# Kernel optimization log

Hardware: AMD Instinct MI355X
Metric: run time of the kernel (lower is better)

Reference implementation:

```python
import jax, jax.numpy as jnp
import numpy as np

RMS_EPS = 1e-6

def rms_norm(x, w, eps=RMS_EPS):
    # LLaMA RMSNorm: x * rsqrt(mean(x^2) + eps) * w
    var = jnp.mean(jnp.square(x), axis=-1, keepdims=True)
    return x * jax.lax.rsqrt(var + eps) * w

def setup_inputs() -> dict:
    key = jax.random.key(0)
    k1, k2, k3 = jax.random.split(key, 3)
    B, S, D, V = 2, 2048, 4096, 32000
    hidden_states = jax.random.normal(k1, (B, S, D), dtype=jnp.float32)
    norm_weight = jnp.ones((D,), dtype=jnp.float32)
    lm_head_weight = jax.random.normal(k2, (V, D), dtype=jnp.float32) * 0.02
    attention_mask = jnp.ones((B, S), dtype=jnp.int32)
    labels = jax.random.randint(k3, (B, S), 0, V, dtype=jnp.int32).astype(jnp.int64)
    return {
        "hidden_states": hidden_states,
        "norm_weight": norm_weight,
        "lm_head_weight": lm_head_weight,
        "attention_mask": attention_mask,
        "labels": labels,
    }

def reference(hidden_states, norm_weight, lm_head_weight, attention_mask, labels):
    B, S, D = hidden_states.shape
    V = lm_head_weight.shape[0]
    h = rms_norm(hidden_states, norm_weight)
    # lm_head: Linear(D -> V, bias=False); cast logits to fp32 (full-vocab tensor)
    logits = jnp.einsum('bsd,vd->bsv', h, lm_head_weight).astype(jnp.float32)
    # shift: drop last logit position / first label position.
    # attention_mask is all-ones here, so the boolean select keeps every row
    # -> static-shape flatten to [B*(S-1), V], matching torch semantics.
    shift_logits = logits[:, :-1, :].reshape(B * (S - 1), V)
    shift_labels = labels[:, 1:].reshape(B * (S - 1))
    return shift_logits, shift_labels
```

## Files before the change

kernel.cpp:

```cpp
#include <hip/hip_runtime.h>
#include <hip/hip_bf16.h>
#include <stdint.h>

#define B_DIM 2
#define S_DIM 2048
#define D_DIM 4096
#define V_DIM 32000
#define M_DIM (B_DIM * S_DIM)
#define OUT_ROWS (B_DIM * (S_DIM-1))

typedef __hip_bfloat16 bf16;
typedef __bf16 bf16x8 __attribute__((ext_vector_type(8)));
typedef float floatx4 __attribute__((ext_vector_type(4)));

__device__ __forceinline__ void async16(const bf16* g, bf16* l) {
    __builtin_amdgcn_global_load_lds(
        (const __attribute__((address_space(1))) void*)g,
        (__attribute__((address_space(3))) void*)l,
        16, 0, 0);
}

__global__ void rmsnorm_cast_kernel(const float* __restrict__ x,
                                    const float* __restrict__ w,
                                    bf16* __restrict__ h) {
    const int row = blockIdx.x;
    const int t = threadIdx.x;
    const float* xr = x + (size_t)row * D_DIM;

    float4 vals[4];
    float ss = 0.f;
#pragma unroll
    for (int i = 0; i < 4; ++i) {
        float4 v = ((const float4*)xr)[t + i * 256];
        vals[i] = v;
        ss += v.x * v.x + v.y * v.y + v.z * v.z + v.w * v.w;
    }
#pragma unroll
    for (int off = 32; off; off >>= 1) ss += __shfl_down(ss, off, 64);
    __shared__ float wsum[4];
    const int lane = t & 63, wv = t >> 6;
    if (lane == 0) wsum[wv] = ss;
    __syncthreads();
    const float var = (wsum[0] + wsum[1] + wsum[2] + wsum[3]) * (1.0f / D_DIM);
    const float scale = rsqrtf(var + 1e-6f);

    bf16* hr = h + (size_t)row * D_DIM;
#pragma unroll
    for (int i = 0; i < 4; ++i) {
        const int f4 = t + i * 256;
        float4 v = vals[i];
        float4 wv4 = ((const float4*)w)[f4];
        ushort4 pk;
        bf16 b0 = __float2bfloat16(v.x * scale * wv4.x);
        bf16 b1 = __float2bfloat16(v.y * scale * wv4.y);
        bf16 b2 = __float2bfloat16(v.z * scale * wv4.z);
        bf16 b3 = __float2bfloat16(v.w * scale * wv4.w);
        pk.x = *(unsigned short*)&b0;
        pk.y = *(unsigned short*)&b1;
        pk.z = *(unsigned short*)&b2;
        pk.w = *(unsigned short*)&b3;
        ((ushort4*)hr)[f4] = pk;
    }
}

__global__ void wcast_kernel(const float* __restrict__ W, bf16* __restrict__ Wb) {
    const size_t i = (size_t)blockIdx.x * 256 + threadIdx.x;
    float4 v = ((const float4*)W)[i];
    ushort4 pk;
    bf16 b0 = __float2bfloat16(v.x);
    bf16 b1 = __float2bfloat16(v.y);
    bf16 b2 = __float2bfloat16(v.z);
    bf16 b3 = __float2bfloat16(v.w);
    pk.x = *(unsigned short*)&b0;
    pk.y = *(unsigned short*)&b1;
    pk.z = *(unsigned short*)&b2;
    pk.w = *(unsigned short*)&b3;
    ((ushort4*)Wb)[i] = pk;
}

#define BM 256
#define BN 256
#define BK 64

#define STAGE_A(db, half, kt) do { \
    const bf16* _g = aRow0 + (size_t)(half) * 128 * D_DIM + (kt) * BK; \
    bf16* _l = lds + (db) * 32768 + (half) * 8192 + t * 8; \
    async16(_g, _l); \
    async16(_g + (size_t)64 * D_DIM, _l + 4096); \
} while (0)

#define STAGE_B(db, half, kt) do { \
    const bf16* _g = bRow0 + (size_t)(half) * 128 * D_DIM + (kt) * BK; \
    bf16* _l = lds + (db) * 32768 + 16384 + (half) * 8192 + t * 8; \
    async16(_g, _l); \
    async16(_g + (size_t)64 * D_DIM, _l + 4096); \
} while (0)

#define LDA(db, mi, ks) (*(const bf16x8*)(lds + (db) * 32768 + aBase + (mi) * 1024 + ((ks) ? csw1 : csw0)))
#define LDB(db, ni, ks) (*(const bf16x8*)(lds + (db) * 32768 + bBase + (ni) * 1024 + ((ks) ? csw1 : csw0)))
#define MFMA(a, b, c) __builtin_amdgcn_mfma_f32_16x16x32_bf16((a), (b), (c), 0, 0, 0)
#define BAR() __builtin_amdgcn_s_barrier()
#define PRIO1() __builtin_amdgcn_s_setprio(1)
#define PRIO0() __builtin_amdgcn_s_setprio(0)

__global__ __launch_bounds__(512, 2) void gemm_kernel(const bf16* __restrict__ A,
                                                      const bf16* __restrict__ Bw,
                                                      float* __restrict__ Cout) {
    __shared__ __align__(16) bf16 lds[65536];

    const int bid = blockIdx.x;
    const int wg  = (bid & 7) * 250 + (bid >> 3);
    const int bm  = wg & 15;
    const int bn  = wg >> 4;
    const int m0  = bm * BM, n0 = bn * BN;

    const int t    = threadIdx.x;
    const int lane = t & 63;
    const int wv   = t >> 6;
    const int wmi  = wv >> 2;
    const int wni  = wv & 3;
    const int quad = lane >> 4;
    const int l15  = lane & 15;

    const int r0 = t >> 3;
    const int c0 = ((t & 7) ^ (r0 & 7)) << 3;
    const bf16* aRow0 = A  + (size_t)(m0 + r0) * D_DIM + c0;
    const bf16* bRow0 = Bw + (size_t)(n0 + r0) * D_DIM + c0;

    const int vx   = (l15 & 7) << 3;
    const int csw0 = ((quad << 3)     ) ^ vx;
    const int csw1 = ((quad << 3) | 32) ^ vx;
    const int aBase = wmi * 8192 + l15 * 64;
    const int bBase = 16384 + (wni >> 1) * 8192 + (wni & 1) * 4096 + l15 * 64;

    floatx4 acc[8][4] = {};
    bf16x8 af[4][2], b01[2][2], b23[2][2];

    STAGE_B(0, 0, 0); STAGE_B(0, 1, 0); STAGE_A(0, 0, 0); STAGE_A(0, 1, 0);
    STAGE_B(1, 0, 1); STAGE_B(1, 1, 1); STAGE_A(1, 0, 1); STAGE_A(1, 1, 1);
    asm volatile("s_waitcnt vmcnt(8)" ::: "memory");
    BAR();

    for (int it = 0; it < 32; ++it) {
        int kta = 2 * it + 2; if (kta > 63) kta = 63;
        int ktb = 2 * it + 3; if (ktb > 63) ktb = 63;

#pragma unroll
        for (int db = 0; db < 2; ++db) {
#pragma unroll
            for (int mi = 0; mi < 4; ++mi) { af[mi][0] = LDA(db, mi, 0); af[mi][1] = LDA(db, mi, 1); }
#pragma unroll
            for (int ni = 0; ni < 2; ++ni) { b01[ni][0] = LDB(db, ni, 0); b01[ni][1] = LDB(db, ni, 1); }
            if (db == 1) STAGE_A(0, 0, kta);
            BAR();
            PRIO1();
#pragma unroll
            for (int mi = 0; mi < 4; ++mi)
#pragma unroll
                for (int ni = 0; ni < 2; ++ni) {
                    acc[mi][ni] = MFMA(af[mi][0], b01[ni][0], acc[mi][ni]);
                    acc[mi][ni] = MFMA(af[mi][1], b01[ni][1], acc[mi][ni]);
                }
            PRIO0();
            BAR();

#pragma unroll
            for (int ni = 0; ni < 2; ++ni) { b23[ni][0] = LDB(db, ni + 2, 0); b23[ni][1] = LDB(db, ni + 2, 1); }
            if (db == 1) STAGE_A(0, 1, kta);
            BAR();
            PRIO1();
#pragma unroll
            for (int mi = 0; mi < 4; ++mi)
#pragma unroll
                for (int ni = 0; ni < 2; ++ni) {
                    acc[mi][ni + 2] = MFMA(af[mi][0], b23[ni][0], acc[mi][ni + 2]);
                    acc[mi][ni + 2] = MFMA(af[mi][1], b23[ni][1], acc[mi][ni + 2]);
                }
            PRIO0();
            BAR();

#pragma unroll
            for (int mi = 0; mi < 4; ++mi) { af[mi][0] = LDA(db, mi + 4, 0); af[mi][1] = LDA(db, mi + 4, 1); }
            if (db == 0) { STAGE_B(0, 0, kta); }
            else         { STAGE_B(1, 0, ktb); STAGE_B(1, 1, ktb); }
            BAR();
            PRIO1();
#pragma unroll
            for (int mi = 0; mi < 4; ++mi)
#pragma unroll
                for (int ni = 0; ni < 2; ++ni) {
                    acc[mi + 4][ni] = MFMA(af[mi][0], b01[ni][0], acc[mi + 4][ni]);
                    acc[mi + 4][ni] = MFMA(af[mi][1], b01[ni][1], acc[mi + 4][ni]);
                }
            PRIO0();
            BAR();

            if (db == 0) { STAGE_B(0, 1, kta); }
            else         { STAGE_A(1, 0, ktb); STAGE_A(1, 1, ktb); }
            BAR();
            PRIO1();
#pragma unroll
            for (int mi = 0; mi < 4; ++mi)
#pragma unroll
                for (int ni = 0; ni < 2; ++ni) {
                    acc[mi + 4][ni + 2] = MFMA(af[mi][0], b23[ni][0], acc[mi + 4][ni + 2]);
                    acc[mi + 4][ni + 2] = MFMA(af[mi][1], b23[ni][1], acc[mi + 4][ni + 2]);
                }
            PRIO0();
            if (db == 0) { asm volatile("s_waitcnt vmcnt(4)" ::: "memory"); }
            else         { asm volatile("s_waitcnt vmcnt(8)" ::: "memory"); }
            BAR();
        }
    }

    const int mbase = m0 + wmi * 128 + quad * 4;
    const int nbase = n0 + wni * 64 + l15;
#pragma unroll
    for (int mi = 0; mi < 8; ++mi) {
#pragma unroll
        for (int r = 0; r < 4; ++r) {
            const int m = mbase + mi * 16 + r;
            const int s = m & (S_DIM - 1);
            if (s == S_DIM - 1) continue;
            float* cp = Cout + (size_t)((m >> 11) * (S_DIM - 1) + s) * V_DIM + nbase;
#pragma unroll
            for (int ni = 0; ni < 4; ++ni)
                cp[ni * 16] = acc[mi][ni][r];
        }
    }
}

__global__ void labels_kernel(const int* __restrict__ labels, float* __restrict__ out) {
    const int r = blockIdx.x * 256 + threadIdx.x;
    if (r >= OUT_ROWS) return;
    const int b = r / (S_DIM - 1);
    const int s = r % (S_DIM - 1);
    out[r] = (float)labels[b * S_DIM + s + 1];
}

extern "C" void kernel_launch(void* const* d_in, const int* in_sizes, int n_in,
                              void* d_out, int out_size, void* d_ws, size_t ws_size,
                              hipStream_t stream) {
    const float* x      = (const float*)d_in[0];
    const float* nw     = (const float*)d_in[1];
    const float* W      = (const float*)d_in[2];
    const int*   labels = (const int*)d_in[4];

    float* logits_out = (float*)d_out;
    float* labels_out = logits_out + (size_t)OUT_ROWS * V_DIM;

    bf16* h  = (bf16*)d_ws;
    bf16* Wb = h + (size_t)M_DIM * D_DIM;

    rmsnorm_cast_kernel<<<M_DIM, 256, 0, stream>>>(x, nw, h);
    wcast_kernel<<<(int)((size_t)V_DIM * D_DIM / 4 / 256), 256, 0, stream>>>(W, Wb);
    gemm_kernel<<<(M_DIM / BM) * (V_DIM / BN), 512, 0, stream>>>(h, Wb, logits_out);
    labels_kernel<<<(OUT_ROWS + 255) / 256, 256, 0, stream>>>(labels, labels_out);
}
```

Measured before the change: 2.328 ms.

## Restructure GEMM mainloop with double-buffered A and triple-buffered B tiles

Replaces the combined double-buffered LDS layout with separate rings: two slots for the A tile and three for the B tile, each holding a full 256x64 tile. The loop now steps one K-tile per iteration and issues all loads for that iteration in its last phase. The B tile is fetched three tiles ahead and A two ahead, with a single vmcnt wait per iteration. This aims to hide more global-load latency. In exchange, LDS use grows to the full 160KB per block and the loads are bunched into one phase instead of spread across the four MFMA phases.

```diff
diff --git a/kernel.cpp b/kernel.cpp
--- a/kernel.cpp
+++ b/kernel.cpp
@@ -81,23 +81,28 @@
 #define BM 256
 #define BN 256
 #define BK 64
-
-#define STAGE_A(db, half, kt) do { \
-    const bf16* _g = aRow0 + (size_t)(half) * 128 * D_DIM + (kt) * BK; \
-    bf16* _l = lds + (db) * 32768 + (half) * 8192 + t * 8; \
-    async16(_g, _l); \
-    async16(_g + (size_t)64 * D_DIM, _l + 4096); \
+#define LDS_TILE 16384
+
+#define STAGE_A(slot, kt) do { \
+    const bf16* _g = aRow0 + (size_t)(kt) * BK; \
+    bf16* _l = ldsA + (slot) * LDS_TILE + t * 8; \
+    async16(_g,                       _l); \
+    async16(_g + (size_t) 64 * D_DIM, _l + 4096); \
+    async16(_g + (size_t)128 * D_DIM, _l + 8192); \
+    async16(_g + (size_t)192 * D_DIM, _l + 12288); \
 } while (0)
 
-#define STAGE_B(db, half, kt) do { \
-    const bf16* _g = bRow0 + (size_t)(half) * 128 * D_DIM + (kt) * BK; \
-    bf16* _l = lds + (db) * 32768 + 16384 + (half) * 8192 + t * 8; \
-    async16(_g, _l); \
-    async16(_g + (size_t)64 * D_DIM, _l + 4096); \
+#define STAGE_B(slot, kt) do { \
+    const bf16* _g = bRow0 + (size_t)(kt) * BK; \
+    bf16* _l = ldsB + (slot) * LDS_TILE + t * 8; \
+    async16(_g,                       _l); \
+    async16(_g + (size_t) 64 * D_DIM, _l + 4096); \
+    async16(_g + (size_t)128 * D_DIM, _l + 8192); \
+    async16(_g + (size_t)192 * D_DIM, _l + 12288); \
 } while (0)
 
-#define LDA(db, mi, ks) (*(const bf16x8*)(lds + (db) * 32768 + aBase + (mi) * 1024 + ((ks) ? csw1 : csw0)))
-#define LDB(db, ni, ks) (*(const bf16x8*)(lds + (db) * 32768 + bBase + (ni) * 1024 + ((ks) ? csw1 : csw0)))
+#define LDA(mi, ks) (*(const bf16x8*)(aT + (mi) * 1024 + aBase + ((ks) ? csw1 : csw0)))
+#define LDB(ni, ks) (*(const bf16x8*)(bT + (ni) * 1024 + bBase + ((ks) ? csw1 : csw0)))
 #define MFMA(a, b, c) __builtin_amdgcn_mfma_f32_16x16x32_bf16((a), (b), (c), 0, 0, 0)
 #define BAR() __builtin_amdgcn_s_barrier()
 #define PRIO1() __builtin_amdgcn_s_setprio(1)
@@ -106,7 +111,8 @@
 __global__ __launch_bounds__(512, 2) void gemm_kernel(const bf16* __restrict__ A,
                                                       const bf16* __restrict__ Bw,
                                                       float* __restrict__ Cout) {
-    __shared__ __align__(16) bf16 lds[65536];
+    __shared__ __align__(16) bf16 ldsA[2 * LDS_TILE];
+    __shared__ __align__(16) bf16 ldsB[3 * LDS_TILE];
 
     const int bid = blockIdx.x;
     const int wg  = (bid & 7) * 250 + (bid >> 3);
@@ -131,86 +137,87 @@
     const int csw0 = ((quad << 3)     ) ^ vx;
     const int csw1 = ((quad << 3) | 32) ^ vx;
     const int aBase = wmi * 8192 + l15 * 64;
-    const int bBase = 16384 + (wni >> 1) * 8192 + (wni & 1) * 4096 + l15 * 64;
+    const int bBase = (wni >> 1) * 8192 + (wni & 1) * 4096 + l15 * 64;
 
     floatx4 acc[8][4] = {};
     bf16x8 af[4][2], b01[2][2], b23[2][2];
 
-    STAGE_B(0, 0, 0); STAGE_B(0, 1, 0); STAGE_A(0, 0, 0); STAGE_A(0, 1, 0);
-    STAGE_B(1, 0, 1); STAGE_B(1, 1, 1); STAGE_A(1, 0, 1); STAGE_A(1, 1, 1);
-    asm volatile("s_waitcnt vmcnt(8)" ::: "memory");
+    STAGE_B(0, 0);
+    STAGE_A(0, 0);
+    STAGE_B(1, 1);
+    STAGE_A(1, 1);
+    STAGE_B(2, 2);
+    asm volatile("s_waitcnt vmcnt(12)" ::: "memory");
     BAR();
 
-    for (int it = 0; it < 32; ++it) {
-        int kta = 2 * it + 2; if (kta > 63) kta = 63;
-        int ktb = 2 * it + 3; if (ktb > 63) ktb = 63;
-
-#pragma unroll
-        for (int db = 0; db < 2; ++db) {
-#pragma unroll
-            for (int mi = 0; mi < 4; ++mi) { af[mi][0] = LDA(db, mi, 0); af[mi][1] = LDA(db, mi, 1); }
-#pragma unroll
-            for (int ni = 0; ni < 2; ++ni) { b01[ni][0] = LDB(db, ni, 0); b01[ni][1] = LDB(db, ni, 1); }
-            if (db == 1) STAGE_A(0, 0, kta);
-            BAR();
-            PRIO1();
-#pragma unroll
-            for (int mi = 0; mi < 4; ++mi)
-#pragma unroll
-                for (int ni = 0; ni < 2; ++ni) {
-                    acc[mi][ni] = MFMA(af[mi][0], b01[ni][0], acc[mi][ni]);
-                    acc[mi][ni] = MFMA(af[mi][1], b01[ni][1], acc[mi][ni]);
-                }
-            PRIO0();
-            BAR();
-
-#pragma unroll
-            for (int ni = 0; ni < 2; ++ni) { b23[ni][0] = LDB(db, ni + 2, 0); b23[ni][1] = LDB(db, ni + 2, 1); }
-            if (db == 1) STAGE_A(0, 1, kta);
-            BAR();
-            PRIO1();
-#pragma unroll
-            for (int mi = 0; mi < 4; ++mi)
-#pragma unroll
-                for (int ni = 0; ni < 2; ++ni) {
-                    acc[mi][ni + 2] = MFMA(af[mi][0], b23[ni][0], acc[mi][ni + 2]);
-                    acc[mi][ni + 2] = MFMA(af[mi][1], b23[ni][1], acc[mi][ni + 2]);
-                }
-            PRIO0();
-            BAR();
-
-#pragma unroll
-            for (int mi = 0; mi < 4; ++mi) { af[mi][0] = LDA(db, mi + 4, 0); af[mi][1] = LDA(db, mi + 4, 1); }
-            if (db == 0) { STAGE_B(0, 0, kta); }
-            else         { STAGE_B(1, 0, ktb); STAGE_B(1, 1, ktb); }
-            BAR();
-            PRIO1();
-#pragma unroll
-            for (int mi = 0; mi < 4; ++mi)
-#pragma unroll
-                for (int ni = 0; ni < 2; ++ni) {
-                    acc[mi + 4][ni] = MFMA(af[mi][0], b01[ni][0], acc[mi + 4][ni]);
-                    acc[mi + 4][ni] = MFMA(af[mi][1], b01[ni][1], acc[mi + 4][ni]);
-                }
-            PRIO0();
-            BAR();
-
-            if (db == 0) { STAGE_B(0, 1, kta); }
-            else         { STAGE_A(1, 0, ktb); STAGE_A(1, 1, ktb); }
-            BAR();
-            PRIO1();
-#pragma unroll
-            for (int mi = 0; mi < 4; ++mi)
-#pragma unroll
-                for (int ni = 0; ni < 2; ++ni) {
-                    acc[mi + 4][ni + 2] = MFMA(af[mi][0], b23[ni][0], acc[mi + 4][ni + 2]);
-                    acc[mi + 4][ni + 2] = MFMA(af[mi][1], b23[ni][1], acc[mi + 4][ni + 2]);
-                }
-            PRIO0();
-            if (db == 0) { asm volatile("s_waitcnt vmcnt(4)" ::: "memory"); }
-            else         { asm volatile("s_waitcnt vmcnt(8)" ::: "memory"); }
-            BAR();
-        }
+    int bs = 0;
+    for (int j = 0; j < 64; ++j) {
+        const int as = j & 1;
+        int ka = j + 2; if (ka > 63) ka = 63;
+        int kb = j + 3; if (kb > 63) kb = 63;
+        const bf16* aT = ldsA + as * LDS_TILE;
+        const bf16* bT = ldsB + bs * LDS_TILE;
+
+#pragma unroll
+        for (int mi = 0; mi < 4; ++mi) { af[mi][0] = LDA(mi, 0); af[mi][1] = LDA(mi, 1); }
+#pragma unroll
+        for (int ni = 0; ni < 2; ++ni) { b01[ni][0] = LDB(ni, 0); b01[ni][1] = LDB(ni, 1); }
+        BAR();
+        PRIO1();
+#pragma unroll
+        for (int mi = 0; mi < 4; ++mi)
+#pragma unroll
+            for (int ni = 0; ni < 2; ++ni) {
+                acc[mi][ni] = MFMA(af[mi][0], b01[ni][0], acc[mi][ni]);
+                acc[mi][ni] = MFMA(af[mi][1], b01[ni][1], acc[mi][ni]);
+            }
+        PRIO0();
+        BAR();
+
+#pragma unroll
+        for (int ni = 0; ni < 2; ++ni) { b23[ni][0] = LDB(ni + 2, 0); b23[ni][1] = LDB(ni + 2, 1); }
+        BAR();
+        PRIO1();
+#pragma unroll
+        for (int mi = 0; mi < 4; ++mi)
+#pragma unroll
+            for (int ni = 0; ni < 2; ++ni) {
+                acc[mi][ni + 2] = MFMA(af[mi][0], b23[ni][0], acc[mi][ni + 2]);
+                acc[mi][ni + 2] = MFMA(af[mi][1], b23[ni][1], acc[mi][ni + 2]);
+            }
+        PRIO0();
+        BAR();
+
+#pragma unroll
+        for (int mi = 0; mi < 4; ++mi) { af[mi][0] = LDA(mi + 4, 0); af[mi][1] = LDA(mi + 4, 1); }
+        BAR();
+        PRIO1();
+#pragma unroll
+        for (int mi = 0; mi < 4; ++mi)
+#pragma unroll
+            for (int ni = 0; ni < 2; ++ni) {
+                acc[mi + 4][ni] = MFMA(af[mi][0], b01[ni][0], acc[mi + 4][ni]);
+                acc[mi + 4][ni] = MFMA(af[mi][1], b01[ni][1], acc[mi + 4][ni]);
+            }
+        PRIO0();
+        BAR();
+
+        STAGE_A(as, ka);
+        STAGE_B(bs, kb);
+        BAR();
+        PRIO1();
+#pragma unroll
+        for (int mi = 0; mi < 4; ++mi)
+#pragma unroll
+            for (int ni = 0; ni < 2; ++ni) {
+                acc[mi + 4][ni + 2] = MFMA(af[mi][0], b23[ni][0], acc[mi + 4][ni + 2]);
+                acc[mi + 4][ni + 2] = MFMA(af[mi][1], b23[ni][1], acc[mi + 4][ni + 2]);
+            }
+        PRIO0();
+        asm volatile("s_waitcnt vmcnt(12)" ::: "memory");
+        BAR();
+
+        bs = (bs == 2) ? 0 : bs + 1;
     }
 
     const int mbase = m0 + wmi * 128 + quad * 4;
```

Result: faster. 2.071 ms (-11.0%).
